# Optimization experiments

Measured on AMD Instinct MI355X. Metric: run time of the kernel, lower is better.

The kernel has to match this reference:

```python
import jax, jax.numpy as jnp
import numpy as np
import math

B, S, HID = 1, 4096, 2048
NH, NKV, HD = 16, 4, 128
SKETCH, TOPK = 640, 2048
EPS = 1e-6


def _dct_orthonormal(rows, cols, rng, sink=4, fsink=8):
    i = np.arange(rows)[:, None]
    j = np.arange(cols)[None, :]
    dct = np.cos(np.pi / cols * (j + 0.5) * i)
    dct[0, :] *= math.sqrt(1.0 / cols)
    dct[1:, :] *= math.sqrt(2.0 / cols)
    signs = rng.integers(0, 2, (1, cols)).astype(np.float64) * 2.0 - 1.0
    m = dct * signs
    m[:, :sink] *= 2.0
    m[:fsink, :] *= 1.5
    return m.astype(np.float32)


def setup_inputs() -> dict:
    key = jax.random.key(0)
    ks = jax.random.split(key, 8)
    rng = np.random.default_rng(0)
    # RoPE tables (b, s, 1, head_dim)
    pos = np.arange(S, dtype=np.float32)
    inv = 1.0 / (10000.0 ** (np.arange(0, HD, 2, dtype=np.float32) / HD))
    ang = pos[:, None] * inv[None, :]              # (S, HD/2)
    emb = np.concatenate([ang, ang], axis=-1)       # (S, HD)
    cos = np.broadcast_to(np.cos(emb)[None, :, None, :], (B, S, 1, HD)).copy()
    sin = np.broadcast_to(np.sin(emb)[None, :, None, :], (B, S, 1, HD)).copy()
    w = 0.02
    return {
        'hidden_states': jax.random.normal(ks[0], (B, S, HID), jnp.float32),
        'wq': jax.random.normal(ks[1], (HID, NH * HD), jnp.float32) * w,
        'wk': jax.random.normal(ks[2], (HID, NKV * HD), jnp.float32) * w,
        'wv': jax.random.normal(ks[3], (HID, NKV * HD), jnp.float32) * w,
        'wo': jax.random.normal(ks[4], (NH * HD, HID), jnp.float32) * w,
        'qn_w': jnp.ones((HD,), jnp.float32),
        'kn_w': jnp.ones((HD,), jnp.float32),
        's_w1': jax.random.normal(ks[5], (HID, 64), jnp.float32) * w,
        's_b1': jnp.zeros((64,), jnp.float32),
        's_w2': jax.random.normal(ks[6], (64, 1), jnp.float32) * w,
        's_b2': jnp.zeros((1,), jnp.float32),
        'sketch_scale': jnp.full((1,), 0.1, jnp.float32),
        'kron_a': jnp.asarray(_dct_orthonormal(20, 128, rng)),
        'kron_b': jnp.asarray(_dct_orthonormal(32, 256, rng)),
        'cos': jnp.asarray(cos),
        'sin': jnp.asarray(sin),
    }


def _rms_norm(x, w):
    var = jnp.mean(jnp.square(x), axis=-1, keepdims=True)
    return x * jax.lax.rsqrt(var + EPS) * w


def _rope(x, cos, sin):
    # x: (b, s, h, d); cos/sin: (b, s, 1, d)
    d2 = x.shape[-1] // 2
    rot = jnp.concatenate([-x[..., d2:], x[..., :d2]], axis=-1)
    return x * cos + rot * sin


def reference(hidden_states, wq, wk, wv, wo, qn_w, kn_w, s_w1, s_b1, s_w2, s_b2,
              sketch_scale, kron_a, kron_b, cos, sin):
    b, s, _ = hidden_states.shape
    # importance scorer with compression pressure bias
    logits = jnp.tanh(hidden_states @ s_w1 + s_b1) @ s_w2 + s_b2   # (b, s, 1)
    if s > SKETCH:
        logits = logits - math.log(s / SKETCH)
    iw = jax.nn.sigmoid(logits)                                    # (b, s, 1)

    q = (hidden_states @ wq).reshape(b, s, NH, HD)
    k = (hidden_states @ wk).reshape(b, s, NKV, HD)
    v = (hidden_states @ wv).reshape(b, s, NKV, HD)
    q = _rms_norm(q, qn_w)
    k = _rms_norm(k, kn_w)

    tk = min(s, TOPK)
    _, idx = jax.lax.top_k(logits[..., 0], tk)                     # (b, tk)
    ix = idx[:, :, None, None]
    k_detail = jnp.take_along_axis(k, ix, axis=1)                  # (b, tk, nkv, d)
    v_detail = jnp.take_along_axis(v, ix, axis=1)
    cos_det = jnp.take_along_axis(cos, ix, axis=1)                 # (b, tk, 1, d)
    sin_det = jnp.take_along_axis(sin, ix, axis=1)

    # Kronecker sketch of importance-weighted K/V over all tokens
    P = jnp.kron(kron_a, kron_b)[:, :s]                            # (640, s)
    kw = k * iw[..., None]
    vw = v * iw[..., None]
    k_sketch = jnp.einsum('bshd,ms->bmhd', kw, P) * sketch_scale
    v_sketch = jnp.einsum('bshd,ms->bmhd', vw, P) * sketch_scale

    q_rope = _rope(q, cos, sin)
    k_detail = _rope(k_detail, cos_det, sin_det)

    k_final = jnp.concatenate([k_detail, k_sketch], axis=1)        # (b, tk+640, nkv, d)
    v_final = jnp.concatenate([v_detail, v_sketch], axis=1)
    rep = NH // NKV
    k_final = jnp.repeat(k_final, rep, axis=2)                     # (b, L, nh, d)
    v_final = jnp.repeat(v_final, rep, axis=2)

    scores = jnp.einsum('bqhd,bkhd->bhqk', q_rope, k_final) / math.sqrt(HD)
    attn = jax.nn.softmax(scores, axis=-1)
    out = jnp.einsum('bhqk,bkhd->bqhd', attn, v_final).reshape(b, s, NH * HD)
    return out @ wo
```

## Files before the change

### kernel.cpp

```cpp
#include <hip/hip_runtime.h>
#include <math.h>

typedef _Float16 f16;
typedef f16 f16x8 __attribute__((ext_vector_type(8)));
typedef float f32x4 __attribute__((ext_vector_type(4)));

#define MFMA16(a,b,c) __builtin_amdgcn_mfma_f32_16x16x32_f16(a,b,c,0,0,0)

static __device__ __forceinline__ f16x8 ld8(const f16* p) { return *(const f16x8*)p; }

static __device__ __forceinline__ float exp2a(float x) {
    float r; asm("v_exp_f32 %0, %1" : "=v"(r) : "v"(x)); return r;
}

#if __has_builtin(__builtin_amdgcn_global_load_lds)
#define GLL16(g, lptr) __builtin_amdgcn_global_load_lds((const __attribute__((address_space(1))) void*)(g), (__attribute__((address_space(3))) void*)(lptr), 16, 0, 0)
#else
#define GLL16(g, lptr) do { *(int4*)(lptr) = *(const int4*)(g); } while (0)
#endif

__global__ __launch_bounds__(256) void k_mlp(const float* __restrict__ h, const float* __restrict__ w1,
                                             const float* __restrict__ b1, const float* __restrict__ w2,
                                             const float* __restrict__ b2, double* __restrict__ logitsD,
                                             float* __restrict__ iw, f16* __restrict__ h16) {
    __shared__ float hl[4 * 2048];
    __shared__ double tl[4][64];
    int tid = threadIdx.x;
    int s0 = blockIdx.x * 4;
    #pragma unroll
    for (int p = 0; p < 8; ++p) {
        int off = p * 1024 + tid * 4;
        *(float4*)&hl[off] = *(const float4*)&h[(size_t)s0 * 2048 + off];
    }
    __syncthreads();
    #pragma unroll
    for (int p = 0; p < 4; ++p) {
        int off = p * 2048 + tid * 8;
        f16x8 v;
        #pragma unroll
        for (int j = 0; j < 8; ++j) v[j] = (f16)hl[off + j];
        *(f16x8*)&h16[(size_t)s0 * 2048 + off] = v;
    }
    int j = tid & 63, r = tid >> 6;
    const float* hr = &hl[r * 2048];
    double acc = 0.0;
    for (int c = 0; c < 2048; ++c) acc += (double)hr[c] * (double)w1[c * 64 + j];
    acc += (double)b1[j];
    tl[r][j] = tanh(acc);
    __syncthreads();
    int lane = tid & 63, rr = tid >> 6;
    double v = tl[rr][lane] * (double)w2[lane];
    for (int o = 32; o > 0; o >>= 1) v += __shfl_down(v, o);
    if (lane == 0) {
        double lg = v + (double)b2[0] - 1.8562979903656263;
        logitsD[s0 + rr] = lg;
        iw[s0 + rr] = (float)(1.0 / (1.0 + exp(-lg)));
    }
}

__global__ __launch_bounds__(256) void k_transpose_qkv(const float* __restrict__ wq, const float* __restrict__ wk,
                                                       const float* __restrict__ wv, f16* __restrict__ out) {
    __shared__ float tile[32][33];
    int bx = blockIdx.x;
    const float* in; int inCols, colBase, rowOff;
    if (bx < 64)      { in = wq; inCols = 2048; colBase = bx * 32;        rowOff = colBase; }
    else if (bx < 80) { in = wk; inCols = 512;  colBase = (bx - 64) * 32; rowOff = 2048 + colBase; }
    else              { in = wv; inCols = 512;  colBase = (bx - 80) * 32; rowOff = 2560 + colBase; }
    int tx = threadIdx.x, ty = threadIdx.y;
    int x = colBase + tx;
    int y0 = blockIdx.y * 32;
    #pragma unroll
    for (int i = 0; i < 4; ++i)
        tile[ty + i*8][tx] = in[(size_t)(y0 + ty + i*8) * inCols + x];
    __syncthreads();
    #pragma unroll
    for (int i = 0; i < 4; ++i)
        out[(size_t)(rowOff + ty + i*8) * 2048 + y0 + tx] = (f16)tile[tx][ty + i*8];
}

__global__ __launch_bounds__(256) void k_transpose(const float* __restrict__ in, f16* __restrict__ out,
                                                   int inCols, int rowOff) {
    __shared__ float tile[32][33];
    int tx = threadIdx.x, ty = threadIdx.y;
    int x = blockIdx.x * 32 + tx;
    int y0 = blockIdx.y * 32;
    #pragma unroll
    for (int i = 0; i < 4; ++i)
        tile[ty + i*8][tx] = in[(size_t)(y0 + ty + i*8) * inCols + x];
    __syncthreads();
    #pragma unroll
    for (int i = 0; i < 4; ++i)
        out[(size_t)(rowOff + blockIdx.x*32 + ty + i*8) * 2048 + y0 + tx] = (f16)tile[tx][ty + i*8];
}

__global__ __launch_bounds__(1024) void k_topk(const double* __restrict__ logitsD, int* __restrict__ sel) {
    __shared__ unsigned long long keys[4096];
    __shared__ unsigned int hist[2048];
    __shared__ unsigned int bcast[2];
    __shared__ unsigned int cA, cB;
    int tid = threadIdx.x;
    for (int i = tid; i < 4096; i += 1024) {
        unsigned long long u = (unsigned long long)__double_as_longlong(logitsD[i]);
        keys[i] = (u >> 63) ? ~u : (u | 0x8000000000000000ull);
    }
    if (tid == 0) { cA = 0; cB = 0; }
    unsigned long long Tpart = 0;
    unsigned int need = 2048;
    #pragma unroll 1
    for (int lvl = 0; lvl < 6; ++lvl) {
        int shift = (lvl < 5) ? (53 - 11*lvl) : 0;
        int width = (lvl < 5) ? 11 : 9;
        unsigned int nb = 1u << width;
        int hiShift = shift + width;
        for (int i = tid; i < (int)nb; i += 1024) hist[i] = 0;
        __syncthreads();
        for (int i = tid; i < 4096; i += 1024) {
            unsigned long long k = keys[i];
            bool cand = (lvl == 0) || ((k >> hiShift) == (Tpart >> hiShift));
            if (cand) atomicAdd(&hist[(unsigned int)(k >> shift) & (nb - 1u)], 1u);
        }
        __syncthreads();
        if (tid < 64) {
            int chunk = (int)nb >> 6;
            int base = (int)nb - (tid + 1) * chunk;
            unsigned int sum = 0;
            for (int j = 0; j < chunk; ++j) sum += hist[base + j];
            unsigned int pre = sum;
            #pragma unroll
            for (int o = 1; o < 64; o <<= 1) {
                unsigned int t = __shfl_up(pre, o);
                if (tid >= o) pre += t;
            }
            unsigned int preEx = pre - sum;
            if (preEx < need && need <= pre) {
                unsigned int cum = preEx;
                for (int j = chunk - 1; j >= 0; --j) {
                    unsigned int c = hist[base + j];
                    if (cum + c >= need) { bcast[0] = (unsigned int)(base + j); bcast[1] = need - cum; break; }
                    cum += c;
                }
            }
        }
        __syncthreads();
        Tpart |= ((unsigned long long)bcast[0]) << shift;
        need = bcast[1];
        __syncthreads();
    }
    unsigned int G = 2048 - need;
    for (int i = tid; i < 4096; i += 1024) {
        unsigned long long k = keys[i];
        if (k > Tpart) { unsigned int p = atomicAdd(&cA, 1u); sel[p] = i; }
        else if (k == Tpart) { unsigned int q = atomicAdd(&cB, 1u); if (q < need) sel[G + q] = i; }
    }
}

__global__ __launch_bounds__(256) void k_gemm(const f16* __restrict__ A, const f16* __restrict__ Bt,
                                              float* __restrict__ C, int M, int N, int K) {
    __shared__ f16 As[128 * 32];
    __shared__ f16 Bs[128 * 32];
    int tid = threadIdx.x;
    int w = tid >> 6, l = tid & 63, lr = l & 15, lg = l >> 4;
    int wr = w >> 1, wc = w & 1;
    int row0 = blockIdx.y * 128, col0 = blockIdx.x * 128;
    f32x4 zero = {0.f, 0.f, 0.f, 0.f};
    f32x4 acc[4][4];
    #pragma unroll
    for (int m = 0; m < 4; ++m)
        #pragma unroll
        for (int n = 0; n < 4; ++n) acc[m][n] = zero;
    for (int k0 = 0; k0 < K; k0 += 32) {
        #pragma unroll
        for (int p = 0; p < 2; ++p) {
            int id = p * 256 + tid;
            int r = id >> 2, c8 = (id & 3) * 8;
            GLL16(&A[(size_t)(row0 + r) * K + k0 + c8], &As[id * 8]);
            GLL16(&Bt[(size_t)(col0 + r) * K + k0 + c8], &Bs[id * 8]);
        }
        __syncthreads();
        f16x8 a[4], b[4];
        #pragma unroll
        for (int m = 0; m < 4; ++m) a[m] = ld8(&As[(wr*64 + m*16 + lr) * 32 + lg*8]);
        #pragma unroll
        for (int n = 0; n < 4; ++n) b[n] = ld8(&Bs[(wc*64 + n*16 + lr) * 32 + lg*8]);
        #pragma unroll
        for (int m = 0; m < 4; ++m)
            #pragma unroll
            for (int n = 0; n < 4; ++n)
                acc[m][n] = MFMA16(a[m], b[n], acc[m][n]);
        __syncthreads();
    }
    #pragma unroll
    for (int m = 0; m < 4; ++m)
        #pragma unroll
        for (int n = 0; n < 4; ++n)
            #pragma unroll
            for (int i = 0; i < 4; ++i)
                C[(size_t)(row0 + wr*64 + m*16 + lg*4 + i) * N + col0 + wc*64 + n*16 + lr] = acc[m][n][i];
}

__global__ __launch_bounds__(320) void k_norm(const float* __restrict__ qkv, const float* __restrict__ qnw,
                                              const float* __restrict__ knw, const float* __restrict__ cosb,
                                              const float* __restrict__ sinb, f16* __restrict__ qr,
                                              float* __restrict__ kn) {
    int s = blockIdx.x;
    int tid = threadIdx.x;
    if (tid < 256) {
        int h = tid >> 4, ln = tid & 15, d0 = ln * 8;
        const float* src = &qkv[(size_t)s * 3072 + h * 128 + d0];
        float4 a = *(const float4*)src, b = *(const float4*)(src + 4);
        float x[8] = {a.x,a.y,a.z,a.w,b.x,b.y,b.z,b.w};
        float ss = 0;
        #pragma unroll
        for (int j = 0; j < 8; ++j) ss += x[j]*x[j];
        ss += __shfl_xor(ss,1); ss += __shfl_xor(ss,2); ss += __shfl_xor(ss,4); ss += __shfl_xor(ss,8);
        float rn = rsqrtf(ss * (1.0f/128.0f) + 1e-6f);
        float xn[8];
        #pragma unroll
        for (int j = 0; j < 8; ++j) xn[j] = x[j] * rn * qnw[d0 + j];
        const float scl = 0.088388347648318447f * 1.4426950408889634f;
        f16x8 o;
        #pragma unroll
        for (int j = 0; j < 8; ++j) {
            float pr = __shfl_xor(xn[j], 8);
            float rot = (ln < 8) ? -pr : pr;
            int d = d0 + j;
            o[j] = (f16)((xn[j]*cosb[s*128 + d] + rot*sinb[s*128 + d]) * scl);
        }
        *(f16x8*)&qr[(size_t)s * 2048 + h * 128 + d0] = o;
    } else {
        int t2 = tid - 256;
        int h = t2 >> 4, ln = t2 & 15, d0 = ln * 8;
        const float* src = &qkv[(size_t)s * 3072 + 2048 + h * 128 + d0];
        float4 a = *(const float4*)src, b = *(const float4*)(src + 4);
        float x[8] = {a.x,a.y,a.z,a.w,b.x,b.y,b.z,b.w};
        float ss = 0;
        #pragma unroll
        for (int j = 0; j < 8; ++j) ss += x[j]*x[j];
        ss += __shfl_xor(ss,1); ss += __shfl_xor(ss,2); ss += __shfl_xor(ss,4); ss += __shfl_xor(ss,8);
        float rn = rsqrtf(ss * (1.0f/128.0f) + 1e-6f);
        float o[8];
        #pragma unroll
        for (int j = 0; j < 8; ++j) o[j] = x[j] * rn * knw[d0 + j];
        float* dst = &kn[(size_t)s*512 + h*128 + d0];
        *(float4*)dst = make_float4(o[0],o[1],o[2],o[3]);
        *(float4*)(dst+4) = make_float4(o[4],o[5],o[6],o[7]);
    }
}

__global__ __launch_bounds__(128) void k_gather(const int* __restrict__ sel, const float* __restrict__ kn,
                                                const float* __restrict__ qkv, const float* __restrict__ cosb,
                                                const float* __restrict__ sinb, f16* __restrict__ Kf,
                                                f16* __restrict__ VfT) {
    int j = blockIdx.x;
    int s = sel[j];
    int t = threadIdx.x;
    float c = cosb[s*128 + t], sn = sinb[s*128 + t];
    #pragma unroll
    for (int h = 0; h < 4; ++h) {
        float x  = kn[(size_t)s*512 + h*128 + t];
        float pr = kn[(size_t)s*512 + h*128 + (t ^ 64)];
        float rot = (t < 64) ? -pr : pr;
        Kf[(size_t)(h*2688 + j) * 128 + t] = (f16)(x*c + rot*sn);
        float v = qkv[(size_t)s*3072 + 2560 + h*128 + t];
        VfT[(size_t)h*128*2688 + (size_t)t*2688 + j] = (f16)v;
    }
}

__global__ __launch_bounds__(256) void k_sketch1(const float* __restrict__ kn, const float* __restrict__ qkv,
                                                 const float* __restrict__ iw, const float* __restrict__ kronb,
                                                 float* __restrict__ T) {
    int mb = blockIdx.x & 31, sa = blockIdx.x >> 5;
    int which = blockIdx.y;
    int c0 = threadIdx.x * 2;
    float a0 = 0, a1 = 0;
    for (int sb = 0; sb < 256; ++sb) {
        int s = sa * 256 + sb;
        float wgt = kronb[mb * 256 + sb] * iw[s];
        const float* src = which ? &qkv[(size_t)s*3072 + 2560] : &kn[(size_t)s*512];
        a0 += wgt * src[c0];
        a1 += wgt * src[c0 + 1];
    }
    float* dst = &T[(size_t)((which*32 + mb)*16 + sa) * 512 + c0];
    dst[0] = a0; dst[1] = a1;
}

__global__ __launch_bounds__(256) void k_sketch2(const float* __restrict__ T, const float* __restrict__ krona,
                                                 const float* __restrict__ sscale, f16* __restrict__ Kf,
                                                 f16* __restrict__ VfT) {
    int m = blockIdx.x;
    int which = blockIdx.y;
    int ma = m >> 5, mb = m & 31;
    int c0 = threadIdx.x * 2;
    float sc = sscale[0];
    float a0 = 0, a1 = 0;
    #pragma unroll
    for (int sa = 0; sa < 16; ++sa) {
        float ka = krona[ma * 128 + sa];
        const float* t = &T[(size_t)((which*32 + mb)*16 + sa) * 512 + c0];
        a0 += ka * t[0];
        a1 += ka * t[1];
    }
    a0 *= sc; a1 *= sc;
    int key = 2048 + m;
    int h0 = c0 >> 7, d = c0 & 127;
    if (which == 0) {
        Kf[(size_t)(h0*2688 + key)*128 + d]     = (f16)a0;
        Kf[(size_t)(h0*2688 + key)*128 + d + 1] = (f16)a1;
    } else {
        VfT[(size_t)h0*128*2688 + (size_t)d*2688 + key]       = (f16)a0;
        VfT[(size_t)h0*128*2688 + (size_t)(d+1)*2688 + key]   = (f16)a1;
    }
}

__global__ __launch_bounds__(256, 2) void k_attn(const f16* __restrict__ qr, const f16* __restrict__ Kf,
                                                 const f16* __restrict__ VfT, f16* __restrict__ out16) {
    __shared__ f16 KT[2][64 * 128];
    __shared__ f16 VT[2][128 * 64];
    __shared__ f16 P[4][32 * 64];
    int qt = blockIdx.x, h = blockIdx.y;
    int kvh = h >> 2;
    int tid = threadIdx.x;
    int w = tid >> 6, l = tid & 63, lr = l & 15, lg = l >> 4;
    int q0 = qt * 128 + w * 32;
    const char* Kb = (const char*)(Kf + (size_t)kvh * 2688 * 128);
    const char* Vb = (const char*)(VfT + (size_t)kvh * 128 * 2688);
    char* Pw = (char*)&P[w][0];

    int koff[4], voff[2];
    #pragma unroll
    for (int c = 0; c < 4; ++c) koff[c] = (c*64 + lg*16) ^ ((lr & 7) << 5);
    #pragma unroll
    for (int kw = 0; kw < 2; ++kw) voff[kw] = (kw*64 + lg*16) ^ ((lr & 7) << 4);
    int psw = (lr & 7) << 4;

    int L0 = tid * 16;

    f16x8 aq[2][4];
    #pragma unroll
    for (int hh = 0; hh < 2; ++hh)
        #pragma unroll
        for (int c = 0; c < 4; ++c)
            aq[hh][c] = ld8(&qr[(size_t)(q0 + hh*16 + lr) * 2048 + h*128 + c*32 + lg*8]);

    f32x4 zero = {0.f,0.f,0.f,0.f};
    f32x4 o0[8], o1[8];
    #pragma unroll
    for (int f = 0; f < 8; ++f) { o0[f] = zero; o1[f] = zero; }
    float m0[4], m1[4], ls0[4], ls1[4];
    #pragma unroll
    for (int i = 0; i < 4; ++i) { m0[i] = -1e30f; m1[i] = -1e30f; ls0[i] = 0.f; ls1[i] = 0.f; }

    #define STAGE(buf, kt)  do {                                                          \
        _Pragma("unroll")                                                                  \
        for (int i_ = 0; i_ < 4; ++i_) {                                                   \
            int L = L0 + i_*4096;                                                          \
            int krow = L >> 8, kbc = L & 255;                                              \
            GLL16(Kb + (size_t)((kt) + krow)*256 + (kbc ^ ((krow & 7) << 5)),              \
                  (char*)&KT[buf][0] + L);                                                 \
            int vd = L >> 7, vbc = L & 127;                                                \
            GLL16(Vb + (size_t)vd*5376 + (size_t)(kt)*2 + (vbc ^ ((vd & 7) << 4)),         \
                  (char*)&VT[buf][0] + L);                                                 \
        }                                                                                  \
    } while (0)

    STAGE(0, 0);
    asm volatile("s_waitcnt vmcnt(0)" ::: "memory");
    __syncthreads();

    for (int t = 0; t < 42; ++t) {
        int cur = t & 1;
        if (t < 41) STAGE(cur ^ 1, (t + 1) * 64);
        const char* Kc = (const char*)&KT[cur][0];
        const char* Vc = (const char*)&VT[cur][0];

        f32x4 s0[4], s1[4];
        #pragma unroll
        for (int tt = 0; tt < 4; ++tt) { s0[tt] = zero; s1[tt] = zero; }
        __builtin_amdgcn_s_setprio(1);
        #pragma unroll
        for (int tt = 0; tt < 4; ++tt) {
            #pragma unroll
            for (int c = 0; c < 4; ++c) {
                f16x8 kb = ld8((const f16*)(Kc + (tt*16 + lr)*256 + koff[c]));
                s0[tt] = MFMA16(aq[0][c], kb, s0[tt]);
                s1[tt] = MFMA16(aq[1][c], kb, s1[tt]);
            }
        }
        __builtin_amdgcn_s_setprio(0);

        float tl0[4], tl1[4];
        bool need = false;
        #pragma unroll
        for (int i = 0; i < 4; ++i) {
            tl0[i] = fmaxf(fmaxf(s0[0][i], s0[1][i]), fmaxf(s0[2][i], s0[3][i]));
            tl1[i] = fmaxf(fmaxf(s1[0][i], s1[1][i]), fmaxf(s1[2][i], s1[3][i]));
            need = need || (tl0[i] > m0[i]+8.f) || (tl1[i] > m1[i]+8.f);
        }
        if (__any(need)) {
            f32x4 cf0, cf1;
            #pragma unroll
            for (int i = 0; i < 4; ++i) {
                float a = tl0[i];
                a = fmaxf(a, __shfl_xor(a, 1)); a = fmaxf(a, __shfl_xor(a, 2));
                a = fmaxf(a, __shfl_xor(a, 4)); a = fmaxf(a, __shfl_xor(a, 8));
                float mn0 = fmaxf(m0[i], a);
                cf0[i] = exp2a(m0[i] - mn0); m0[i] = mn0; ls0[i] *= cf0[i];
                float b = tl1[i];
                b = fmaxf(b, __shfl_xor(b, 1)); b = fmaxf(b, __shfl_xor(b, 2));
                b = fmaxf(b, __shfl_xor(b, 4)); b = fmaxf(b, __shfl_xor(b, 8));
                float mn1 = fmaxf(m1[i], b);
                cf1[i] = exp2a(m1[i] - mn1); m1[i] = mn1; ls1[i] *= cf1[i];
            }
            #pragma unroll
            for (int f = 0; f < 8; ++f) { o0[f] *= cf0; o1[f] *= cf1; }
        }
        #pragma unroll
        for (int tt = 0; tt < 4; ++tt)
            #pragma unroll
            for (int i = 0; i < 4; ++i) {
                int r0 = lg*4 + i;
                float p0 = exp2a(s0[tt][i] - m0[i]);
                ls0[i] += p0;
                *(f16*)(Pw + ((r0*128 + (tt*16+lr)*2) ^ ((r0 & 7) << 4))) = (f16)p0;
                int r1 = 16 + r0;
                float p1 = exp2a(s1[tt][i] - m1[i]);
                ls1[i] += p1;
                *(f16*)(Pw + ((r1*128 + (tt*16+lr)*2) ^ ((r1 & 7) << 4))) = (f16)p1;
            }
        asm volatile("s_waitcnt lgkmcnt(0)" ::: "memory");
        __builtin_amdgcn_sched_barrier(0);

        __builtin_amdgcn_s_setprio(1);
        #pragma unroll
        for (int kw = 0; kw < 2; ++kw) {
            f16x8 pa0 = *(const f16x8*)(Pw + ((lr*128 + kw*64 + lg*16) ^ psw));
            f16x8 pa1 = *(const f16x8*)(Pw + (((16+lr)*128 + kw*64 + lg*16) ^ psw));
            #pragma unroll
            for (int f = 0; f < 8; ++f) {
                f16x8 vb = ld8((const f16*)(Vc + (f*16 + lr)*128 + voff[kw]));
                o0[f] = MFMA16(pa0, vb, o0[f]);
                o1[f] = MFMA16(pa1, vb, o1[f]);
            }
        }
        __builtin_amdgcn_s_setprio(0);
        asm volatile("s_waitcnt vmcnt(0)" ::: "memory");
        __syncthreads();
    }

    #pragma unroll
    for (int i = 0; i < 4; ++i) {
        float a = ls0[i];
        a += __shfl_xor(a, 1); a += __shfl_xor(a, 2); a += __shfl_xor(a, 4); a += __shfl_xor(a, 8);
        float inv0 = 1.0f / a;
        float b = ls1[i];
        b += __shfl_xor(b, 1); b += __shfl_xor(b, 2); b += __shfl_xor(b, 4); b += __shfl_xor(b, 8);
        float inv1 = 1.0f / b;
        #pragma unroll
        for (int f = 0; f < 8; ++f) {
            out16[(size_t)(q0 + lg*4 + i) * 2048 + h*128 + f*16 + lr]      = (f16)(o0[f][i] * inv0);
            out16[(size_t)(q0 + 16 + lg*4 + i) * 2048 + h*128 + f*16 + lr] = (f16)(o1[f][i] * inv1);
        }
    }
    #undef STAGE
}

extern "C" void kernel_launch(void* const* d_in, const int* in_sizes, int n_in,
                              void* d_out, int out_size, void* d_ws, size_t ws_size,
                              hipStream_t stream) {
    const float* h     = (const float*)d_in[0];
    const float* wq    = (const float*)d_in[1];
    const float* wk    = (const float*)d_in[2];
    const float* wv    = (const float*)d_in[3];
    const float* wo    = (const float*)d_in[4];
    const float* qnw   = (const float*)d_in[5];
    const float* knw   = (const float*)d_in[6];
    const float* sw1   = (const float*)d_in[7];
    const float* sb1   = (const float*)d_in[8];
    const float* sw2   = (const float*)d_in[9];
    const float* sb2   = (const float*)d_in[10];
    const float* sscal = (const float*)d_in[11];
    const float* ka    = (const float*)d_in[12];
    const float* kb    = (const float*)d_in[13];
    const float* cosb  = (const float*)d_in[14];
    const float* sinb  = (const float*)d_in[15];
    float* outp = (float*)d_out;

    char* ws = (char*)d_ws;
    size_t off = 0;
    f16*    h16    = (f16*)(ws + off);   off += (size_t)4096*2048*2;
    f16*    wqkvt  = (f16*)(ws + off);   off += (size_t)3072*2048*2;
    f16*    wot    = (f16*)(ws + off);   off += (size_t)2048*2048*2;
    float*  qkvraw = (float*)(ws + off); off += (size_t)4096*3072*4;
    f16*    qr     = (f16*)(ws + off);   off += (size_t)4096*2048*2;
    float*  kn     = (float*)(ws + off); off += (size_t)4096*512*4;
    f16*    attn16 = (f16*)(ws + off);   off += (size_t)4096*2048*2;
    float*  T      = (float*)(ws + off); off += (size_t)2*32*16*512*4;
    f16*    Kf     = (f16*)(ws + off);   off += (size_t)4*2688*128*2;
    f16*    VfT    = (f16*)(ws + off);   off += (size_t)4*128*2688*2;
    double* logitsD= (double*)(ws + off);off += (size_t)4096*8;
    float*  iw     = (float*)(ws + off); off += (size_t)4096*4;
    int*    sel    = (int*)(ws + off);   off += (size_t)2048*4;

    k_mlp<<<1024, 256, 0, stream>>>(h, sw1, sb1, sw2, sb2, logitsD, iw, h16);
    k_transpose_qkv<<<dim3(96,64), dim3(32,8), 0, stream>>>(wq, wk, wv, wqkvt);
    k_transpose<<<dim3(64,64), dim3(32,8), 0, stream>>>(wo, wot, 2048, 0);
    k_topk<<<1, 1024, 0, stream>>>(logitsD, sel);
    k_gemm<<<dim3(24,32), 256, 0, stream>>>(h16, wqkvt, qkvraw, 4096, 3072, 2048);
    k_norm<<<4096, 320, 0, stream>>>(qkvraw, qnw, knw, cosb, sinb, qr, kn);
    k_gather<<<2048, 128, 0, stream>>>(sel, kn, qkvraw, cosb, sinb, Kf, VfT);
    k_sketch1<<<dim3(512,2), 256, 0, stream>>>(kn, qkvraw, iw, kb, T);
    k_sketch2<<<dim3(640,2), 256, 0, stream>>>(T, ka, sscal, Kf, VfT);
    k_attn<<<dim3(32,16), 256, 0, stream>>>(qr, Kf, VfT, attn16);
    k_gemm<<<dim3(16,32), 256, 0, stream>>>(attn16, wot, outp, 4096, 2048, 2048);
}
```

Before: 432.2 us.

## Tile scoring MLP as register-blocked fp64 GEMM with split-K reduction kernel

Replaces the per-4-row scoring MLP kernel, where each thread streamed the full w1 column from global memory, with a tiled GEMM. It uses 64x64 shared-memory tiles, 4x4 fp64 register blocking, split-K over 4 slices and register prefetch of the next chunk. A second small kernel sums the partials, applies tanh and the output layer, and reuses the qkvraw buffer for the partials. The aim is to cut redundant w1 global reads and raise arithmetic reuse. The cost is an extra launch and a round-trip of the partials through global memory.

```diff
diff --git a/kernel.cpp b/kernel.cpp
--- a/kernel.cpp
+++ b/kernel.cpp
@@ -19,42 +19,97 @@
 #define GLL16(g, lptr) do { *(int4*)(lptr) = *(const int4*)(g); } while (0)
 #endif
 
-__global__ __launch_bounds__(256) void k_mlp(const float* __restrict__ h, const float* __restrict__ w1,
-                                             const float* __restrict__ b1, const float* __restrict__ w2,
-                                             const float* __restrict__ b2, double* __restrict__ logitsD,
-                                             float* __restrict__ iw, f16* __restrict__ h16) {
-    __shared__ float hl[4 * 2048];
-    __shared__ double tl[4][64];
+__global__ __launch_bounds__(256) void k_mlp1(const float* __restrict__ h, const float* __restrict__ w1,
+                                              double* __restrict__ part, f16* __restrict__ h16) {
+    __shared__ float hs[64 * 68];
+    __shared__ float ws[64 * 64];
+    int rb = blockIdx.x, ks = blockIdx.y;
     int tid = threadIdx.x;
-    int s0 = blockIdx.x * 4;
-    #pragma unroll
-    for (int p = 0; p < 8; ++p) {
-        int off = p * 1024 + tid * 4;
-        *(float4*)&hl[off] = *(const float4*)&h[(size_t)s0 * 2048 + off];
-    }
-    __syncthreads();
-    #pragma unroll
-    for (int p = 0; p < 4; ++p) {
-        int off = p * 2048 + tid * 8;
-        f16x8 v;
-        #pragma unroll
-        for (int j = 0; j < 8; ++j) v[j] = (f16)hl[off + j];
-        *(f16x8*)&h16[(size_t)s0 * 2048 + off] = v;
-    }
-    int j = tid & 63, r = tid >> 6;
-    const float* hr = &hl[r * 2048];
-    double acc = 0.0;
-    for (int c = 0; c < 2048; ++c) acc += (double)hr[c] * (double)w1[c * 64 + j];
-    acc += (double)b1[j];
-    tl[r][j] = tanh(acc);
-    __syncthreads();
-    int lane = tid & 63, rr = tid >> 6;
-    double v = tl[rr][lane] * (double)w2[lane];
+    int jq = tid & 15, rt = tid >> 4;
+    double acc[4][4];
+    #pragma unroll
+    for (int r = 0; r < 4; ++r)
+        #pragma unroll
+        for (int q = 0; q < 4; ++q) acc[r][q] = 0.0;
+
+    float4 hreg[4], wreg[4];
+    int hrow[4], hcq[4], wc[4], wq[4];
+    #pragma unroll
+    for (int i = 0; i < 4; ++i) {
+        int fl = i * 256 + tid;
+        hrow[i] = fl >> 4; hcq[i] = fl & 15;
+        wc[i] = fl >> 4;   wq[i] = fl & 15;
+    }
+    #define LOADCH(c8) do {                                                                  \
+        _Pragma("unroll")                                                                     \
+        for (int i = 0; i < 4; ++i) {                                                         \
+            hreg[i] = *(const float4*)&h[(size_t)(rb*64 + hrow[i])*2048 + ks*512 + (c8)*64 + hcq[i]*4]; \
+            wreg[i] = *(const float4*)&w1[(size_t)(ks*512 + (c8)*64 + wc[i])*64 + wq[i]*4];   \
+        }                                                                                     \
+    } while (0)
+
+    LOADCH(0);
+    for (int c8 = 0; c8 < 8; ++c8) {
+        __syncthreads();
+        #pragma unroll
+        for (int i = 0; i < 4; ++i) {
+            *(float4*)&hs[hrow[i]*68 + hcq[i]*4] = hreg[i];
+            *(float4*)&ws[wc[i]*64 + wq[i]*4] = wreg[i];
+            const float* hp = (const float*)&hreg[i];
+            f16 h4[4];
+            #pragma unroll
+            for (int z = 0; z < 4; ++z) h4[z] = (f16)hp[z];
+            *(float*)&h16[(size_t)(rb*64 + hrow[i])*2048 + ks*512 + c8*64 + hcq[i]*4] = *(float*)h4;
+            *(float*)(&h16[(size_t)(rb*64 + hrow[i])*2048 + ks*512 + c8*64 + hcq[i]*4 + 2]) = *(((float*)h4)+1);
+        }
+        __syncthreads();
+        if (c8 < 7) LOADCH(c8 + 1);
+        #pragma unroll 4
+        for (int cg = 0; cg < 64; cg += 4) {
+            float4 ha[4], wa[4];
+            #pragma unroll
+            for (int r = 0; r < 4; ++r) ha[r] = *(const float4*)&hs[(rt + 16*r)*68 + cg];
+            #pragma unroll
+            for (int cc = 0; cc < 4; ++cc) wa[cc] = *(const float4*)&ws[(cg + cc)*64 + jq*4];
+            #pragma unroll
+            for (int cc = 0; cc < 4; ++cc) {
+                const float* wap = (const float*)&wa[cc];
+                double wd0 = (double)wap[0], wd1 = (double)wap[1], wd2 = (double)wap[2], wd3 = (double)wap[3];
+                #pragma unroll
+                for (int r = 0; r < 4; ++r) {
+                    double hv = (double)((const float*)&ha[r])[cc];
+                    acc[r][0] = fma(hv, wd0, acc[r][0]);
+                    acc[r][1] = fma(hv, wd1, acc[r][1]);
+                    acc[r][2] = fma(hv, wd2, acc[r][2]);
+                    acc[r][3] = fma(hv, wd3, acc[r][3]);
+                }
+            }
+        }
+    }
+    #pragma unroll
+    for (int r = 0; r < 4; ++r)
+        #pragma unroll
+        for (int q = 0; q < 4; ++q)
+            part[((size_t)ks*4096 + rb*64 + rt + 16*r)*64 + jq*4 + q] = acc[r][q];
+    #undef LOADCH
+}
+
+__global__ __launch_bounds__(256) void k_mlp2(const double* __restrict__ part, const float* __restrict__ b1,
+                                              const float* __restrict__ w2, const float* __restrict__ b2,
+                                              double* __restrict__ logitsD, float* __restrict__ iw) {
+    int tid = threadIdx.x;
+    int j = tid & 63, rq = tid >> 6;
+    int row = blockIdx.x * 4 + rq;
+    double s = part[(size_t)row*64 + j] + part[((size_t)4096 + row)*64 + j]
+             + part[((size_t)8192 + row)*64 + j] + part[((size_t)12288 + row)*64 + j];
+    double t = tanh(s + (double)b1[j]);
+    double v = t * (double)w2[j];
+    #pragma unroll
     for (int o = 32; o > 0; o >>= 1) v += __shfl_down(v, o);
-    if (lane == 0) {
+    if (j == 0) {
         double lg = v + (double)b2[0] - 1.8562979903656263;
-        logitsD[s0 + rr] = lg;
-        iw[s0 + rr] = (float)(1.0 / (1.0 + exp(-lg)));
+        logitsD[row] = lg;
+        iw[row] = (float)(1.0 / (1.0 + exp(-lg)));
     }
 }
 
@@ -124,7 +179,7 @@
             int chunk = (int)nb >> 6;
             int base = (int)nb - (tid + 1) * chunk;
             unsigned int sum = 0;
-            for (int j = 0; j < chunk; ++j) sum += hist[base + j];
+            for (int jj = 0; jj < chunk; ++jj) sum += hist[base + jj];
             unsigned int pre = sum;
             #pragma unroll
             for (int o = 1; o < 64; o <<= 1) {
@@ -134,9 +189,9 @@
             unsigned int preEx = pre - sum;
             if (preEx < need && need <= pre) {
                 unsigned int cum = preEx;
-                for (int j = chunk - 1; j >= 0; --j) {
-                    unsigned int c = hist[base + j];
-                    if (cum + c >= need) { bcast[0] = (unsigned int)(base + j); bcast[1] = need - cum; break; }
+                for (int jj = chunk - 1; jj >= 0; --jj) {
+                    unsigned int c = hist[base + jj];
+                    if (cum + c >= need) { bcast[0] = (unsigned int)(base + jj); bcast[1] = need - cum; break; }
                     cum += c;
                 }
             }
@@ -500,8 +555,10 @@
     double* logitsD= (double*)(ws + off);off += (size_t)4096*8;
     float*  iw     = (float*)(ws + off); off += (size_t)4096*4;
     int*    sel    = (int*)(ws + off);   off += (size_t)2048*4;
-
-    k_mlp<<<1024, 256, 0, stream>>>(h, sw1, sb1, sw2, sb2, logitsD, iw, h16);
+    double* part   = (double*)qkvraw;
+
+    k_mlp1<<<dim3(64,4), 256, 0, stream>>>(h, sw1, part, h16);
+    k_mlp2<<<1024, 256, 0, stream>>>(part, sb1, sw2, sb2, logitsD, iw);
     k_transpose_qkv<<<dim3(96,64), dim3(32,8), 0, stream>>>(wq, wk, wv, wqkvt);
     k_transpose<<<dim3(64,64), dim3(32,8), 0, stream>>>(wo, wot, 2048, 0);
     k_topk<<<1, 1024, 0, stream>>>(logitsD, sel);
```

Result: faster. 415.7 us (-3.8%).
